# Optimization experiments

Hardware: AMD Instinct MI355X
Metric: run time of the kernel (lower is better)

Reference implementation:

```python
import jax, jax.numpy as jnp
import numpy as np

N_NODES = 100000


def gcn_conv(x, W, b, src, dst, n_nodes):
    # PyG GCNConv: h = x @ W; add self-loops; norm = d^-1/2[src] * d^-1/2[dst];
    # aggregate sum of norm * h[src] at dst; then + bias.
    h = x @ W  # [N, F_out]
    loops = jnp.arange(n_nodes, dtype=src.dtype)
    s = jnp.concatenate([src, loops])  # [E+N]
    d = jnp.concatenate([dst, loops])
    deg = jax.ops.segment_sum(jnp.ones_like(d, dtype=h.dtype), d, num_segments=n_nodes)
    dinv = jax.lax.rsqrt(deg)  # deg >= 1 thanks to self-loops
    norm = dinv[s] * dinv[d]  # [E+N]
    msg = h[s] * norm[:, None]  # [E+N, F_out] -- large gather
    out = jax.ops.segment_sum(msg, d, num_segments=n_nodes)  # scatter-add
    return out + b


def setup_inputs() -> dict:
    key = jax.random.key(0)
    k = jax.random.split(key, 8)
    x = jax.random.normal(k[0], (N_NODES, 8), dtype=jnp.float32)
    edge_index = jax.random.randint(k[1], (2, 1600000), 0, N_NODES, dtype=jnp.int32)
    W1 = jax.random.normal(k[2], (8, 64), dtype=jnp.float32) * 0.3
    b1 = jnp.zeros((64,), dtype=jnp.float32)
    W2 = jax.random.normal(k[3], (64, 128), dtype=jnp.float32) * 0.1
    b2 = jnp.zeros((128,), dtype=jnp.float32)
    Wfc = jax.random.normal(k[4], (128, 1), dtype=jnp.float32) * 0.08
    bfc = jnp.zeros((1,), dtype=jnp.float32)
    return {"x": x, "edge_index": edge_index, "W1": W1, "b1": b1,
            "W2": W2, "b2": b2, "Wfc": Wfc, "bfc": bfc}


def reference(x, edge_index, W1, b1, W2, b2, Wfc, bfc):
    src, dst = edge_index[0], edge_index[1]
    n = x.shape[0]
    h = jax.nn.relu(gcn_conv(x, W1, b1, src, dst, n))   # dropout: eval mode (identity)
    h = jax.nn.relu(gcn_conv(h, W2, b2, src, dst, n))
    g = jnp.mean(h, axis=0)  # [128] graph readout
    return g @ Wfc + bfc     # [1]
```

## Files before the change

kernel.cpp:

```cpp
#include <hip/hip_runtime.h>


#define CHUNK 4096
#define NB_SHIFT 8
#define BCAP 5120
#define G2_GRID 1042

typedef float v2f __attribute__((ext_vector_type(2)));
typedef __bf16 bf16x8 __attribute__((ext_vector_type(8)));
typedef float f32x16 __attribute__((ext_vector_type(16)));

__device__ __forceinline__ unsigned short f2bf(float f) {
    unsigned u = __float_as_uint(f);
    return (unsigned short)((u + 0x7fffu + ((u >> 16) & 1u)) >> 16);
}
__device__ __forceinline__ unsigned pkbf(float a, float b) {
    return ((unsigned)f2bf(b) << 16) | f2bf(a);
}
__device__ __forceinline__ float bflo(unsigned u) { return __uint_as_float(u << 16); }
__device__ __forceinline__ float bfhi(unsigned u) { return __uint_as_float(u & 0xffff0000u); }
__device__ __forceinline__ bf16x8 asbf8(uint4 v) { return __builtin_bit_cast(bf16x8, v); }

__global__ __launch_bounds__(512) void scatterA(const int* __restrict__ ei, int E,
                                                int* __restrict__ cursor,
                                                unsigned int* __restrict__ bucketed) {
    __shared__ unsigned int pk[CHUNK];
    __shared__ unsigned short bk[CHUNK];
    __shared__ unsigned int spk[CHUNK];
    __shared__ unsigned short sbk[CHUNK];
    __shared__ int h[512], hsc[512], lcur[512], rbase[512];
    int tid = threadIdx.x;
    h[tid] = 0;
    lcur[tid] = 0;
    __syncthreads();
    int cbase = blockIdx.x * CHUNK;
    int cN = min(CHUNK, E - cbase);
    const int* src = ei;
    const int* dst = ei + E;
    for (int i = tid; i < cN; i += 512) {
        int s = src[cbase + i], d = dst[cbase + i];
        int b = d >> NB_SHIFT;
        pk[i] = (unsigned)s | ((unsigned)(d & 255) << 17);
        bk[i] = (unsigned short)b;
        atomicAdd(&h[b], 1);
    }
    __syncthreads();
    hsc[tid] = h[tid];
    __syncthreads();
    for (int off = 1; off < 512; off <<= 1) {
        int v0 = (tid >= off) ? hsc[tid - off] : 0;
        __syncthreads();
        hsc[tid] += v0;
        __syncthreads();
    }
    hsc[tid] -= h[tid];
    if (h[tid]) rbase[tid] = tid * BCAP + atomicAdd(&cursor[tid], h[tid]);
    __syncthreads();
    for (int i = tid; i < cN; i += 512) {
        int b = bk[i];
        int pos = hsc[b] + atomicAdd(&lcur[b], 1);
        spk[pos] = pk[i];
        sbk[pos] = (unsigned short)b;
    }
    __syncthreads();
    for (int p = tid; p < cN; p += 512) {
        int b = sbk[p];
        bucketed[rbase[b] + (p - hsc[b])] = spk[p];
    }
}

__global__ __launch_bounds__(512) void buildB(
    const unsigned int* __restrict__ bucketed, const int* __restrict__ cursor,
    int* __restrict__ row_start, int* __restrict__ cntg, float* __restrict__ dinv,
    int* __restrict__ csr_src, const float* __restrict__ x,
    unsigned int* __restrict__ xsb, int n) {
    __shared__ unsigned int spk[BCAP];
    __shared__ int scsr[BCAP];
    __shared__ int cnt[256], sc[256], cur[256];
    __shared__ float sdinv[256];
    int tid = threadIdx.x;
    int b = blockIdx.x;
    int s0 = b * BCAP;
    int m = cursor[b];
    if (tid < 256) cnt[tid] = 0;
    __syncthreads();
    for (int e = tid; e < m; e += 512) {
        unsigned v = bucketed[s0 + e];
        spk[e] = v;
        atomicAdd(&cnt[v >> 17], 1);
    }
    __syncthreads();
    if (tid < 256) sc[tid] = cnt[tid];
    __syncthreads();
    for (int off = 1; off < 256; off <<= 1) {
        int v0 = (tid < 256 && tid >= off) ? sc[tid - off] : 0;
        __syncthreads();
        if (tid < 256) sc[tid] += v0;
        __syncthreads();
    }
    int nb0 = b << NB_SHIFT;
    if (tid < 256) {
        int node = nb0 + tid;
        int ex = sc[tid] - cnt[tid];
        cur[tid] = ex;
        float dv = rsqrtf((float)cnt[tid] + 1.0f);
        sdinv[tid] = dv;
        if (node < n) {
            row_start[node] = s0 + ex;
            cntg[node] = cnt[tid];
            dinv[node] = dv;
        }
    }
    __syncthreads();
    for (int e = tid; e < m; e += 512) {
        unsigned v = spk[e];
        int r = atomicAdd(&cur[v >> 17], 1);
        scsr[r] = (int)(v & 0x1FFFFu);
    }
    __syncthreads();
    for (int e = tid; e < m; e += 512) csr_src[s0 + e] = scsr[e];
    int lim = min(n - nb0, 256) * 4;
    for (int i = tid; i < lim; i += 512) {
        float2 v = ((const float2*)x)[nb0 * 4 + i];
        float dvv = sdinv[i >> 2];
        xsb[nb0 * 4 + i] = pkbf(v.x * dvv, v.y * dvv);
    }
}

__global__ __launch_bounds__(256) void aggX_gemm1(
    const unsigned int* __restrict__ xsb, const float* __restrict__ dinv,
    const int* __restrict__ row_start, const int* __restrict__ cnt,
    const int* __restrict__ csr_src, const float* __restrict__ W1,
    const float* __restrict__ b1, unsigned int* __restrict__ h1q, int n) {
    __shared__ float w[512 + 64];
    __shared__ float axl[64 * 8];
    __shared__ float sdi[64];
    int tid = threadIdx.x;
    for (int i = tid; i < 512; i += 256) w[i] = W1[i];
    if (tid < 64) w[512 + tid] = b1[tid];
    int g = tid >> 2, l = tid & 3;
    int node = blockIdx.x * 64 + g;
    float a[8] = {};
    float di = 0.f;
    if (node < n) {
        di = dinv[node];
        const uint4* xs4 = (const uint4*)xsb;
        int e0 = row_start[node], e1 = e0 + cnt[node];
        int e = e0 + l;
        for (; e + 4 < e1; e += 8) {
            int sA = csr_src[e], sB = csr_src[e + 4];
            uint4 uA = xs4[sA], uB = xs4[sB];
            a[0] += bflo(uA.x) + bflo(uB.x);
            a[1] += bfhi(uA.x) + bfhi(uB.x);
            a[2] += bflo(uA.y) + bflo(uB.y);
            a[3] += bfhi(uA.y) + bfhi(uB.y);
            a[4] += bflo(uA.z) + bflo(uB.z);
            a[5] += bfhi(uA.z) + bfhi(uB.z);
            a[6] += bflo(uA.w) + bflo(uB.w);
            a[7] += bfhi(uA.w) + bfhi(uB.w);
        }
        for (; e < e1; e += 4) {
            uint4 u = xs4[csr_src[e]];
            a[0] += bflo(u.x); a[1] += bfhi(u.x);
            a[2] += bflo(u.y); a[3] += bfhi(u.y);
            a[4] += bflo(u.z); a[5] += bfhi(u.z);
            a[6] += bflo(u.w); a[7] += bfhi(u.w);
        }
        if (l == 0) {
            uint4 u = xs4[node];
            a[0] += bflo(u.x); a[1] += bfhi(u.x);
            a[2] += bflo(u.y); a[3] += bfhi(u.y);
            a[4] += bflo(u.z); a[5] += bfhi(u.z);
            a[6] += bflo(u.w); a[7] += bfhi(u.w);
        }
    }
#pragma unroll
    for (int k = 0; k < 8; k++) {
        a[k] += __shfl_xor(a[k], 1);
        a[k] += __shfl_xor(a[k], 2);
    }
    axl[g * 8 + 2 * l] = di * a[2 * l];
    axl[g * 8 + 2 * l + 1] = di * a[2 * l + 1];
    if (l == 0) sdi[g] = di;
    __syncthreads();
    int wv = tid >> 6, lane = tid & 63;
    int nb = blockIdx.x * 64;
    for (int it = 0; it < 16; it++) {
        int nl = wv * 16 + it;
        int nd = nb + nl;
        if (nd >= n) break;
        float h = w[512 + lane];
#pragma unroll
        for (int k = 0; k < 8; k++) h = fmaf(axl[nl * 8 + k], w[k * 64 + lane], h);
        float h1s = fmaxf(h, 0.f) * sdi[nl];
        unsigned word = ((unsigned)__builtin_amdgcn_cvt_pk_fp8_f32(h1s, h1s, 0, false)
                         & 0xFFu) << ((lane & 3) * 8);
        word |= __shfl_xor((int)word, 1);
        word |= __shfl_xor((int)word, 2);
        if ((lane & 3) == 0) h1q[nd * 16 + (lane >> 2)] = word;
    }
}

__global__ void agg64(const unsigned int* __restrict__ h1q, const float* __restrict__ dinv,
                      const int* __restrict__ row_start, const int* __restrict__ cnt,
                      const int* __restrict__ csr_src, uint2* __restrict__ ahb, int n) {
    int gid = blockIdx.x * blockDim.x + threadIdx.x;
    int node = gid >> 4;
    if (node >= n) return;
    int cq = threadIdx.x & 15;
    int es = cq >> 2, qp = cq & 3;
    const uint4* h4 = (const uint4*)h1q;
    float a[16] = {};
    int e0 = row_start[node], e1 = e0 + cnt[node];
    int e = e0 + es;
    for (; e + 4 < e1; e += 8) {
        int sA = csr_src[e], sB = csr_src[e + 4];
        uint4 uA = h4[sA * 4 + qp], uB = h4[sB * 4 + qp];
#pragma unroll
        for (int wdx = 0; wdx < 4; wdx++) {
            unsigned wa = (&uA.x)[wdx], wb = (&uB.x)[wdx];
            v2f la = __builtin_amdgcn_cvt_pk_f32_fp8((int)wa, false);
            v2f ha = __builtin_amdgcn_cvt_pk_f32_fp8((int)wa, true);
            v2f lb = __builtin_amdgcn_cvt_pk_f32_fp8((int)wb, false);
            v2f hb = __builtin_amdgcn_cvt_pk_f32_fp8((int)wb, true);
            a[wdx * 4 + 0] += la[0] + lb[0];
            a[wdx * 4 + 1] += la[1] + lb[1];
            a[wdx * 4 + 2] += ha[0] + hb[0];
            a[wdx * 4 + 3] += ha[1] + hb[1];
        }
    }
    for (; e < e1; e += 4) {
        uint4 u = h4[csr_src[e] * 4 + qp];
#pragma unroll
        for (int wdx = 0; wdx < 4; wdx++) {
            unsigned wu = (&u.x)[wdx];
            v2f lo = __builtin_amdgcn_cvt_pk_f32_fp8((int)wu, false);
            v2f hi = __builtin_amdgcn_cvt_pk_f32_fp8((int)wu, true);
            a[wdx * 4 + 0] += lo[0];
            a[wdx * 4 + 1] += lo[1];
            a[wdx * 4 + 2] += hi[0];
            a[wdx * 4 + 3] += hi[1];
        }
    }
    if (es == 0) {
        uint4 u = h4[node * 4 + qp];
#pragma unroll
        for (int wdx = 0; wdx < 4; wdx++) {
            unsigned wu = (&u.x)[wdx];
            v2f lo = __builtin_amdgcn_cvt_pk_f32_fp8((int)wu, false);
            v2f hi = __builtin_amdgcn_cvt_pk_f32_fp8((int)wu, true);
            a[wdx * 4 + 0] += lo[0];
            a[wdx * 4 + 1] += lo[1];
            a[wdx * 4 + 2] += hi[0];
            a[wdx * 4 + 3] += hi[1];
        }
    }
#pragma unroll
    for (int k = 0; k < 16; k++) {
        a[k] += __shfl_xor(a[k], 4);
        a[k] += __shfl_xor(a[k], 8);
    }
    if (es == 0) {
        float di = dinv[node];
        uint4 r0, r1;
        r0.x = pkbf(di * a[0], di * a[1]);
        r0.y = pkbf(di * a[2], di * a[3]);
        r0.z = pkbf(di * a[4], di * a[5]);
        r0.w = pkbf(di * a[6], di * a[7]);
        r1.x = pkbf(di * a[8], di * a[9]);
        r1.y = pkbf(di * a[10], di * a[11]);
        r1.z = pkbf(di * a[12], di * a[13]);
        r1.w = pkbf(di * a[14], di * a[15]);
        uint4* out4 = (uint4*)ahb;
        out4[node * 8 + qp * 2] = r0;
        out4[node * 8 + qp * 2 + 1] = r1;
    }
}

__global__ __launch_bounds__(256) void gemm2_fused(
    const uint2* __restrict__ ahb, const float* __restrict__ W2,
    const float* __restrict__ b2, float* __restrict__ partial, int n) {
    __shared__ __align__(16) uint4 wb4[4 * 4 * 64];
    __shared__ __align__(16) uint4 atp4[32 * 8];
    int tid = threadIdx.x;
    unsigned* wbd = (unsigned*)wb4;
    for (int i = tid; i < 4096; i += 256) {
        int j = i & 127;
        int r = i >> 7;
        int t = r >> 3, l5s = (r >> 2) & 1, d = r & 3;
        int k0 = 16 * t + 8 * l5s + 2 * d;
        unsigned val = pkbf(W2[k0 * 128 + j], W2[(k0 + 1) * 128 + j]);
        int w = j >> 5, lan = l5s * 32 + (j & 31);
        wbd[(((w * 4 + t) * 64) + lan) * 4 + d] = val;
    }
    __syncthreads();
    int lane = tid & 63;
    int w = tid >> 6;
    int col = lane & 31;
    int l5 = lane >> 5;
    uint4 bf0 = wb4[(w * 4 + 0) * 64 + lane];
    uint4 bf1 = wb4[(w * 4 + 1) * 64 + lane];
    uint4 bf2 = wb4[(w * 4 + 2) * 64 + lane];
    uint4 bf3 = wb4[(w * 4 + 3) * 64 + lane];
    float bj = b2[w * 32 + col];
    const uint4* ahb4 = (const uint4*)ahb;
    float colsum = 0.f;
    int ntiles = (n + 31) >> 5;
    for (int tt = blockIdx.x; tt < ntiles; tt += gridDim.x) {
        int base = tt * 32;
        __syncthreads();
        {
            int nl = tid >> 3, s = tid & 7;
            uint4 v = make_uint4(0u, 0u, 0u, 0u);
            if (base + nl < n) v = ahb4[(base + nl) * 8 + s];
            atp4[nl * 8 + (s ^ (nl & 7))] = v;
        }
        __syncthreads();
        f32x16 acc = {};
        {
            uint4 a0 = atp4[col * 8 + ((2 * 0 + l5) ^ (col & 7))];
            acc = __builtin_amdgcn_mfma_f32_32x32x16_bf16(asbf8(a0), asbf8(bf0), acc, 0, 0, 0);
            uint4 a1 = atp4[col * 8 + ((2 * 1 + l5) ^ (col & 7))];
            acc = __builtin_amdgcn_mfma_f32_32x32x16_bf16(asbf8(a1), asbf8(bf1), acc, 0, 0, 0);
            uint4 a2 = atp4[col * 8 + ((2 * 2 + l5) ^ (col & 7))];
            acc = __builtin_amdgcn_mfma_f32_32x32x16_bf16(asbf8(a2), asbf8(bf2), acc, 0, 0, 0);
            uint4 a3 = atp4[col * 8 + ((2 * 3 + l5) ^ (col & 7))];
            acc = __builtin_amdgcn_mfma_f32_32x32x16_bf16(asbf8(a3), asbf8(bf3), acc, 0, 0, 0);
        }
        int nvalid = n - base;
        if (nvalid >= 32) {
#pragma unroll
            for (int reg = 0; reg < 16; reg++) colsum += fmaxf(acc[reg] + bj, 0.f);
        } else {
#pragma unroll
            for (int reg = 0; reg < 16; reg++) {
                int rrow = (reg & 3) + 8 * (reg >> 2) + 4 * l5;
                if (rrow < nvalid) colsum += fmaxf(acc[reg] + bj, 0.f);
            }
        }
    }
    colsum += __shfl_xor(colsum, 32);
    if (l5 == 0) partial[blockIdx.x * 128 + w * 32 + col] = colsum;
}

__global__ __launch_bounds__(1024) void finish_kernel(
    const float* __restrict__ partial, const float* __restrict__ Wfc,
    const float* __restrict__ bfc, float* __restrict__ out, float invN) {
    __shared__ float sh[1024 + 2];
    int tid = threadIdx.x;
    int c = tid & 127, g = tid >> 7;
    float s = 0.f;
#pragma unroll 8
    for (int b = g; b < G2_GRID; b += 8) s += partial[b * 128 + c];
    sh[tid] = s;
    __syncthreads();
    if (tid < 512) sh[tid] += sh[tid + 512];
    __syncthreads();
    if (tid < 256) sh[tid] += sh[tid + 256];
    __syncthreads();
    if (tid < 128) {
        float v = (sh[tid] + sh[tid + 128]) * Wfc[tid];
#pragma unroll
        for (int off = 32; off > 0; off >>= 1) v += __shfl_down(v, off);
        if ((tid & 63) == 0) sh[1024 + (tid >> 6)] = v;
    }
    __syncthreads();
    if (tid == 0) out[0] = (sh[1024] + sh[1025]) * invN + bfc[0];
}

extern "C" void kernel_launch(void* const* d_in, const int* in_sizes, int n_in,
                              void* d_out, int out_size, void* d_ws, size_t ws_size,
                              hipStream_t stream) {
    const float* x   = (const float*)d_in[0];
    const int* ei    = (const int*)d_in[1];
    const float* W1  = (const float*)d_in[2];
    const float* b1  = (const float*)d_in[3];
    const float* W2  = (const float*)d_in[4];
    const float* b2  = (const float*)d_in[5];
    const float* Wfc = (const float*)d_in[6];
    const float* bfc = (const float*)d_in[7];
    float* out = (float*)d_out;

    const int n = in_sizes[0] / 8;
    const int E = in_sizes[1] / 2;

    const int nA = (E + CHUNK - 1) / CHUNK;
    const int B = (n + 255) >> NB_SHIFT;

    char* ws = (char*)d_ws;
    size_t off = 0;
    auto alloc = [&](size_t bytes) -> char* {
        char* p = ws + off;
        off = (off + bytes + 255) & ~(size_t)255;
        return p;
    };
    int*            cursor    = (int*)alloc(512 * 4);
    unsigned int*   bucketed  = (unsigned int*)alloc((size_t)B * BCAP * 4);
    int*            row_start = (int*)alloc((size_t)n * 4);
    int*            cnt       = (int*)alloc((size_t)n * 4);
    float*          dinv      = (float*)alloc((size_t)n * 4);
    int*            csr_src   = (int*)alloc((size_t)B * BCAP * 4);
    unsigned int*   xsb       = (unsigned int*)alloc((size_t)n * 16);
    unsigned int*   h1q       = (unsigned int*)alloc((size_t)n * 64);
    uint2*          ahb       = (uint2*)alloc((size_t)n * 128);
    float*          partial   = (float*)alloc((size_t)G2_GRID * 128 * 4);
    (void)ws_size;

    hipMemsetAsync(cursor, 0, 512 * 4, stream);
    scatterA<<<nA, 512, 0, stream>>>(ei, E, cursor, bucketed);
    buildB<<<B, 512, 0, stream>>>(bucketed, cursor, row_start, cnt, dinv, csr_src,
                                  x, xsb, n);
    aggX_gemm1<<<(n + 63) / 64, 256, 0, stream>>>(xsb, dinv, row_start, cnt, csr_src,
                                                  W1, b1, h1q, n);
    agg64<<<(n * 16 + 255) / 256, 256, 0, stream>>>(h1q, dinv, row_start, cnt, csr_src,
                                                    ahb, n);
    gemm2_fused<<<G2_GRID, 256, 0, stream>>>(ahb, W2, b2, partial, n);
    finish_kernel<<<1, 1024, 0, stream>>>(partial, Wfc, bfc, out, 1.0f / (float)n);
}
```

Measured before the change: 162.7 us.

## Split 64-feature aggregation into two half-feature passes; fold Wfc dot into gemm2

The 64-wide fp8 aggregation now runs as two launches, each covering half of the feature columns. Within each launch, 8 threads split a node's edge list instead of 4, with an extra shuffle stage to reduce across them. The aim is to raise edge-level parallelism and shrink the per-pass gather footprint, at the cost of reading the CSR indices and row metadata twice. Separately, gemm2 now multiplies its column sums by Wfc and reduces them to one scalar per block, so the finish kernel only sums about a thousand floats instead of a 1042x128 partial array.

```diff
diff --git a/kernel.cpp b/kernel.cpp
--- a/kernel.cpp
+++ b/kernel.cpp
@@ -203,18 +203,20 @@
 
 __global__ void agg64(const unsigned int* __restrict__ h1q, const float* __restrict__ dinv,
                       const int* __restrict__ row_start, const int* __restrict__ cnt,
-                      const int* __restrict__ csr_src, uint2* __restrict__ ahb, int n) {
+                      const int* __restrict__ csr_src, uint2* __restrict__ ahb, int n,
+                      int p) {
     int gid = blockIdx.x * blockDim.x + threadIdx.x;
     int node = gid >> 4;
     if (node >= n) return;
     int cq = threadIdx.x & 15;
-    int es = cq >> 2, qp = cq & 3;
+    int es = cq >> 1;
+    int qp = 2 * p + (cq & 1);
     const uint4* h4 = (const uint4*)h1q;
     float a[16] = {};
     int e0 = row_start[node], e1 = e0 + cnt[node];
     int e = e0 + es;
-    for (; e + 4 < e1; e += 8) {
-        int sA = csr_src[e], sB = csr_src[e + 4];
+    for (; e + 8 < e1; e += 16) {
+        int sA = csr_src[e], sB = csr_src[e + 8];
         uint4 uA = h4[sA * 4 + qp], uB = h4[sB * 4 + qp];
 #pragma unroll
         for (int wdx = 0; wdx < 4; wdx++) {
@@ -229,7 +231,7 @@
             a[wdx * 4 + 3] += ha[1] + hb[1];
         }
     }
-    for (; e < e1; e += 4) {
+    for (; e < e1; e += 8) {
         uint4 u = h4[csr_src[e] * 4 + qp];
 #pragma unroll
         for (int wdx = 0; wdx < 4; wdx++) {
@@ -257,6 +259,7 @@
     }
 #pragma unroll
     for (int k = 0; k < 16; k++) {
+        a[k] += __shfl_xor(a[k], 2);
         a[k] += __shfl_xor(a[k], 4);
         a[k] += __shfl_xor(a[k], 8);
     }
@@ -279,9 +282,11 @@
 
 __global__ __launch_bounds__(256) void gemm2_fused(
     const uint2* __restrict__ ahb, const float* __restrict__ W2,
-    const float* __restrict__ b2, float* __restrict__ partial, int n) {
+    const float* __restrict__ b2, const float* __restrict__ Wfc,
+    float* __restrict__ partial, int n) {
     __shared__ __align__(16) uint4 wb4[4 * 4 * 64];
     __shared__ __align__(16) uint4 atp4[32 * 8];
+    __shared__ float wsum[4];
     int tid = threadIdx.x;
     unsigned* wbd = (unsigned*)wb4;
     for (int i = tid; i < 4096; i += 256) {
@@ -340,32 +345,26 @@
         }
     }
     colsum += __shfl_xor(colsum, 32);
-    if (l5 == 0) partial[blockIdx.x * 128 + w * 32 + col] = colsum;
-}
-
-__global__ __launch_bounds__(1024) void finish_kernel(
-    const float* __restrict__ partial, const float* __restrict__ Wfc,
-    const float* __restrict__ bfc, float* __restrict__ out, float invN) {
-    __shared__ float sh[1024 + 2];
+    float v = (l5 == 0) ? colsum * Wfc[w * 32 + col] : 0.f;
+#pragma unroll
+    for (int off = 1; off < 64; off <<= 1) v += __shfl_xor(v, off);
+    if (lane == 0) wsum[w] = v;
+    __syncthreads();
+    if (tid == 0) partial[blockIdx.x] = wsum[0] + wsum[1] + wsum[2] + wsum[3];
+}
+
+__global__ __launch_bounds__(256) void finish_kernel(
+    const float* __restrict__ partial, const float* __restrict__ bfc,
+    float* __restrict__ out, float invN, int G) {
+    __shared__ float sh[4];
     int tid = threadIdx.x;
-    int c = tid & 127, g = tid >> 7;
     float s = 0.f;
-#pragma unroll 8
-    for (int b = g; b < G2_GRID; b += 8) s += partial[b * 128 + c];
-    sh[tid] = s;
-    __syncthreads();
-    if (tid < 512) sh[tid] += sh[tid + 512];
-    __syncthreads();
-    if (tid < 256) sh[tid] += sh[tid + 256];
-    __syncthreads();
-    if (tid < 128) {
-        float v = (sh[tid] + sh[tid + 128]) * Wfc[tid];
-#pragma unroll
-        for (int off = 32; off > 0; off >>= 1) v += __shfl_down(v, off);
-        if ((tid & 63) == 0) sh[1024 + (tid >> 6)] = v;
-    }
-    __syncthreads();
-    if (tid == 0) out[0] = (sh[1024] + sh[1025]) * invN + bfc[0];
+    for (int b = tid; b < G; b += 256) s += partial[b];
+#pragma unroll
+    for (int off = 32; off > 0; off >>= 1) s += __shfl_down(s, off);
+    if ((tid & 63) == 0) sh[tid >> 6] = s;
+    __syncthreads();
+    if (tid == 0) out[0] = (sh[0] + sh[1] + sh[2] + sh[3]) * invN + bfc[0];
 }
 
 extern "C" void kernel_launch(void* const* d_in, const int* in_sizes, int n_in,
@@ -386,6 +385,7 @@
 
     const int nA = (E + CHUNK - 1) / CHUNK;
     const int B = (n + 255) >> NB_SHIFT;
+    const int g64 = (n * 16 + 255) / 256;
 
     char* ws = (char*)d_ws;
     size_t off = 0;
@@ -403,7 +403,7 @@
     unsigned int*   xsb       = (unsigned int*)alloc((size_t)n * 16);
     unsigned int*   h1q       = (unsigned int*)alloc((size_t)n * 64);
     uint2*          ahb       = (uint2*)alloc((size_t)n * 128);
-    float*          partial   = (float*)alloc((size_t)G2_GRID * 128 * 4);
+    float*          partial   = (float*)alloc((size_t)G2_GRID * 4);
     (void)ws_size;
 
     hipMemsetAsync(cursor, 0, 512 * 4, stream);
@@ -412,8 +412,8 @@
                                   x, xsb, n);
     aggX_gemm1<<<(n + 63) / 64, 256, 0, stream>>>(xsb, dinv, row_start, cnt, csr_src,
                                                   W1, b1, h1q, n);
-    agg64<<<(n * 16 + 255) / 256, 256, 0, stream>>>(h1q, dinv, row_start, cnt, csr_src,
-                                                    ahb, n);
-    gemm2_fused<<<G2_GRID, 256, 0, stream>>>(ahb, W2, b2, partial, n);
-    finish_kernel<<<1, 1024, 0, stream>>>(partial, Wfc, bfc, out, 1.0f / (float)n);
-}
+    agg64<<<g64, 256, 0, stream>>>(h1q, dinv, row_start, cnt, csr_src, ahb, n, 0);
+    agg64<<<g64, 256, 0, stream>>>(h1q, dinv, row_start, cnt, csr_src, ahb, n, 1);
+    gemm2_fused<<<G2_GRID, 256, 0, stream>>>(ahb, W2, b2, Wfc, partial, n);
+    finish_kernel<<<1, 256, 0, stream>>>(partial, bfc, out, 1.0f / (float)n, G2_GRID);
+}
```

Measured after the change: 176.3 us. +8.4%, slower.
